# Kernel tuning notes

Measured on AMD Instinct MI355X. Metric: run time of the kernel, lower is better.

The kernel has to match this reference:

```python
import jax, jax.numpy as jnp
import numpy as np

B, S, D = 1, 2048, 1536
H, HD = 24, 64
WINDOW = 512
N_ANCHORS = 4
THETA = 10000.0


def _rope(x):
    # x: [B, H, S, hd] -- matches torch code applied on (B*H, S, hd) with offset=0
    hd = x.shape[-1]
    inv_freq = 1.0 / (THETA ** (jnp.arange(0, hd, 2, dtype=jnp.float32) / hd))
    t = jnp.arange(x.shape[2], dtype=jnp.float32)
    freqs = jnp.outer(t, inv_freq)                      # [S, hd//2]
    emb = jnp.concatenate([freqs, freqs], axis=-1)      # [S, hd]
    cos, sin = jnp.cos(emb), jnp.sin(emb)
    x_rot = jnp.concatenate([-x[..., hd // 2:], x[..., : hd // 2]], axis=-1)
    return x * cos + x_rot * sin


def setup_inputs() -> dict:
    key = jax.random.key(0)
    kx, km, kq, kk, kv = jax.random.split(key, 5)
    std = 0.02
    return {
        "x": jax.random.normal(kx, (B, S, D), jnp.float32),
        "spike_mask": jax.random.bernoulli(km, 0.5, (B, S)),
        "Wq": jax.random.normal(kq, (D, D), jnp.float32) * std,
        "Wk": jax.random.normal(kk, (D, D), jnp.float32) * std,
        "Wv": jax.random.normal(kv, (D, D), jnp.float32) * std,
    }


def reference(x, spike_mask, Wq, Wk, Wv):
    Bq, Sq, Dd = x.shape
    # QKV projections (nn.Linear, bias=False: y = x @ W.T), split heads -> [B, H, S, hd]
    Q = jnp.einsum('bsd,ed->bse', x, Wq).reshape(Bq, Sq, H, HD).transpose(0, 2, 1, 3)
    K = jnp.einsum('bsd,ed->bse', x, Wk).reshape(Bq, Sq, H, HD).transpose(0, 2, 1, 3)
    V = jnp.einsum('bsd,ed->bse', x, Wv).reshape(Bq, Sq, H, HD).transpose(0, 2, 1, 3)
    Q = _rope(Q)
    K = _rope(K)

    # structured mask: causal & (within window | global anchor columns)
    pos = jnp.arange(Sq)
    dist = pos[:, None] - pos[None, :]
    attn_mask = (dist >= 0) & ((dist <= WINDOW) | (pos[None, :] < N_ANCHORS))  # [S, S]

    full_mask = attn_mask[None, None] & spike_mask[:, None, None, :]  # [B,1,S,S]
    query_has_any_key = jnp.any(full_mask, axis=-1, keepdims=True)    # [B,1,S,1]
    safe_mask = full_mask | ~query_has_any_key

    scale = HD ** -0.5
    scores = jnp.einsum('bhqd,bhkd->bhqk', Q, K) * scale
    weights = jax.nn.softmax(jnp.where(safe_mask, scores, -jnp.inf), axis=-1)
    out = jnp.einsum('bhqk,bhkd->bhqd', weights, V)
    out = jnp.where(query_has_any_key, out, 0.0)

    out = out.transpose(0, 2, 1, 3).reshape(Bq, Sq, Dd)
    return out * spike_mask[..., None].astype(out.dtype)
```

## Files before the change

### kernel.cpp

```cpp
#include <hip/hip_runtime.h>
#include <cstdint>
#include <cstddef>

#define S_LEN   2048
#define D_MODEL 1536
#define NH      24
#define HDIM    64
#define WINDOW  512
#define NANCH   4

typedef __attribute__((ext_vector_type(8))) short short8;
typedef __attribute__((ext_vector_type(4))) float floatx4;

#define ASYNC_COPY16(g, l) \
    __builtin_amdgcn_global_load_lds((const __attribute__((address_space(1))) uint32_t*)(g), \
                                     (__attribute__((address_space(3))) uint32_t*)(l), 16, 0, 0)

static __device__ __forceinline__ ushort f32_to_bf16(float f) {
    uint32_t u = __float_as_uint(f);
    uint32_t r = (u + 0x7FFFu + ((u >> 16) & 1u)) >> 16;
    return (ushort)r;
}

__global__ __launch_bounds__(256) void convert_prep_kernel(
    const float* __restrict__ x,
    const float* __restrict__ wq, const float* __restrict__ wk, const float* __restrict__ wv,
    const uint8_t* __restrict__ raw,
    ushort* __restrict__ xb, ushort* __restrict__ wb,
    float* __restrict__ normf, float* __restrict__ cs,
    int xq4, int wq4) {
    const int which = blockIdx.y;
    if (which == 4) {
        if (blockIdx.x < 256) {
            int idx = blockIdx.x * 256 + threadIdx.x;
            int s = idx >> 5, i = idx & 31;
            float inv_freq = expf(-(float)i * 0.2878231366242557f);
            float c, sn;
            sincosf((float)s * inv_freq, &sn, &c);
            cs[s * 64 + i]      = c;
            cs[s * 64 + 32 + i] = sn;
            return;
        }
        if (blockIdx.x != 256) return;
        __shared__ int sh[2];
        if (threadIdx.x == 0) { sh[0] = 0; sh[1] = 0; }
        __syncthreads();
        int f = 0, nz = 0;
        for (int i = threadIdx.x; i < S_LEN; i += 256) {
            uint8_t b = raw[i];
            if ((i & 3) == 3 && b == 0x3f) f++;
            if ((i & 3) != 0 && b != 0)    nz++;
        }
        if (f)  atomicAdd(&sh[0], f);
        if (nz) atomicAdd(&sh[1], nz);
        __syncthreads();
        const int mode = (sh[0] > 0) ? 2 : ((sh[1] > 0) ? 1 : 0);
        for (int i = threadIdx.x; i < S_LEN; i += 256) {
            int v;
            if (mode == 2)      v = (((const float*)raw)[i] != 0.0f) ? 1 : 0;
            else if (mode == 1) v = raw[i] ? 1 : 0;
            else                v = (((const int*)raw)[i] != 0) ? 1 : 0;
            normf[i] = v ? 1.0f : 0.0f;
        }
        return;
    }
    const size_t w_elems = (size_t)D_MODEL * D_MODEL;
    const float* src; ushort* dst; int n4;
    if (which == 0)      { src = x;  dst = xb;               n4 = xq4; }
    else if (which == 1) { src = wq; dst = wb;               n4 = wq4; }
    else if (which == 2) { src = wk; dst = wb + w_elems;     n4 = wq4; }
    else                 { src = wv; dst = wb + 2 * w_elems; n4 = wq4; }
    int i = blockIdx.x * blockDim.x + threadIdx.x;
    if (i >= n4) return;
    float4 v = ((const float4*)src)[i];
    ushort4 o;
    o.x = f32_to_bf16(v.x);
    o.y = f32_to_bf16(v.y);
    o.z = f32_to_bf16(v.z);
    o.w = f32_to_bf16(v.w);
    ((ushort4*)dst)[i] = o;
}

__global__ __launch_bounds__(256) void gemm_qkv_kernel(
    const ushort* __restrict__ xb,
    const ushort* __restrict__ wb,
    const float*  __restrict__ cs,
    ushort* __restrict__ Qf, ushort* __restrict__ Kf, ushort* __restrict__ Vf)
{
    const int lb  = blockIdx.x;
    const int idx = (lb & 7) * 72 + (lb >> 3);
    const int z   = idx / 192;
    const int rem = idx % 192;
    const int n2  = rem >> 4;
    const int tm  = rem & 15;
    const ushort* W = wb + (size_t)z * (D_MODEL * (size_t)D_MODEL);

    __shared__ __align__(16) char smem[32768];

    const int tid  = threadIdx.x;
    const int wave = tid >> 6;
    const int lane = tid & 63;

    const int scol = ((lane & 3) ^ ((lane >> 3) & 3)) * 8;
    const int arow = wave * 32 + (lane >> 2);
    const ushort* gA0 = xb + (size_t)(tm * 128 + arow) * D_MODEL + scol;
    const ushort* gA1 = gA0 + (size_t)16 * D_MODEL;
    const ushort* gB0 = W  + (size_t)(n2 * 128 + arow) * D_MODEL + scol;
    const ushort* gB1 = gB0 + (size_t)16 * D_MODEL;

    const int wm = (wave >> 1) * 64;
    const int wn = (wave & 1) * 64;
    const int lrow  = lane & 15;
    const int quad  = lane >> 4;
    const int xq = (quad ^ ((lrow >> 1) & 3)) * 8;

    floatx4 acc[4][4];
#pragma unroll
    for (int i = 0; i < 4; ++i)
#pragma unroll
        for (int j = 0; j < 4; ++j)
            acc[i][j] = (floatx4){0.f, 0.f, 0.f, 0.f};

    auto STAGE = [&](int b, int kt) {
        ushort* lA = (ushort*)(smem + b * 16384) + wave * 1024;
        ushort* lB = lA + 4096;
        const int ko = kt * 32;
        ASYNC_COPY16(gA0 + ko, lA);
        ASYNC_COPY16(gA1 + ko, lA + 512);
        ASYNC_COPY16(gB0 + ko, lB);
        ASYNC_COPY16(gB1 + ko, lB + 512);
    };

    auto COMPUTE = [&](int b) {
        const ushort* Ah = (const ushort*)(smem + b * 16384);
        const ushort* Bh = Ah + 4096;
        short8 af[4], bf[4];
#pragma unroll
        for (int i = 0; i < 4; ++i) af[i] = *(const short8*)(&Ah[(wm + i * 16 + lrow) * 32 + xq]);
#pragma unroll
        for (int j = 0; j < 4; ++j) bf[j] = *(const short8*)(&Bh[(wn + j * 16 + lrow) * 32 + xq]);
#pragma unroll
        for (int i = 0; i < 4; ++i)
#pragma unroll
            for (int j = 0; j < 4; ++j)
                acc[i][j] = __builtin_amdgcn_mfma_f32_16x16x32_bf16(af[i], bf[j], acc[i][j], 0, 0, 0);
    };

    STAGE(0, 0);
    __syncthreads();

    int cur = 0;
    for (int kt = 0; kt < D_MODEL / 32 - 1; ++kt) {
        STAGE(cur ^ 1, kt + 1);
        COMPUTE(cur);
        __syncthreads();
        cur ^= 1;
    }
    COMPUTE(cur);

    __syncthreads();
    ushort* Lw = (ushort*)(smem + wave * 5120);

    const int r0 = (lane >> 4) * 4;
    const int c0 = lane & 15;
    const int l16  = lane & 15;
    const int h  = n2 * 2 + (wave & 1);
    const int s0 = tm * 128 + wm;

    if (z < 2) {
        const float qscale = (z == 0) ? 0.18033688011112042f : 1.0f;
        ushort* O = (z == 0) ? Qf : Kf;
#pragma unroll
        for (int cc = 0; cc < 2; ++cc) {
#pragma unroll
            for (int i2 = 0; i2 < 2; ++i2) {
                const int i = cc * 2 + i2;
#pragma unroll
                for (int jj = 0; jj < 2; ++jj) {
                    const int cl = jj * 16 + c0;
#pragma unroll
                    for (int r = 0; r < 4; ++r) {
                        const int row = s0 + i * 16 + r0 + r;
                        const float c  = cs[row * 64 + cl];
                        const float sn = cs[row * 64 + 32 + cl];
                        const float x0 = acc[i][jj][r];
                        const float x1 = acc[i][jj + 2][r];
                        const int rl = i2 * 16 + r0 + r;
                        Lw[rl * 72 + cl]      = f32_to_bf16((x0 * c - x1 * sn) * qscale);
                        Lw[rl * 72 + cl + 32] = f32_to_bf16((x1 * c + x0 * sn) * qscale);
                    }
                }
            }
            const int t16base = tm * 8 + (wave >> 1) * 4 + cc * 2;
#pragma unroll
            for (int t = 0; t < 2; ++t) {
#pragma unroll
                for (int p = 0; p < 2; ++p) {
                    uint4 v = *(uint4*)&Lw[(t * 16 + l16) * 72 + p * 32 + quad * 8];
                    *(uint4*)&O[((((size_t)h * 128 + t16base + t) * 2 + p) * 64 + lane) * 8] = v;
                }
            }
            if (cc == 0) __syncthreads();
        }
    } else {
#pragma unroll
        for (int cc = 0; cc < 2; ++cc) {
#pragma unroll
            for (int i2 = 0; i2 < 2; ++i2) {
                const int i = cc * 2 + i2;
#pragma unroll
                for (int j = 0; j < 4; ++j) {
                    const int dl = j * 16 + c0;
                    ushort4 o;
                    o.x = f32_to_bf16(acc[i][j][0]);
                    o.y = f32_to_bf16(acc[i][j][1]);
                    o.z = f32_to_bf16(acc[i][j][2]);
                    o.w = f32_to_bf16(acc[i][j][3]);
                    *(ushort4*)&Lw[dl * 40 + i2 * 16 + r0] = o;
                }
            }
            const int kc = tm * 4 + (wave >> 1) * 2 + cc;
#pragma unroll
            for (int j2 = 0; j2 < 4; ++j2) {
                uint4 v = *(uint4*)&Lw[(j2 * 16 + l16) * 40 + quad * 8];
                *(uint4*)&Vf[((((size_t)h * 64 + kc) * 4 + j2) * 64 + lane) * 8] = v;
            }
            if (cc == 0) __syncthreads();
        }
    }
}

__global__ __launch_bounds__(256) void flash_attn_kernel(
    const ushort* __restrict__ Qf,
    const ushort* __restrict__ Kf,
    const ushort* __restrict__ Vf,
    const float* __restrict__ spikef,
    float* __restrict__ out)
{
    const int lb   = blockIdx.x + (blockIdx.y << 7);
    const int h    = (lb & 7) * 3 + ((lb >> 3) >> 7);
    const int qt16 = (lb >> 3) & 127;
    const int qs   = qt16 * 16;
    const int tid  = threadIdx.x;
    const int wid  = tid >> 6;
    const int lane = tid & 63;
    const int quad = lane >> 4;
    const int l16  = lane & 15;

    __shared__ __align__(16) char smem[4 * 4608];
    char* wreg = smem + wid * 4608;
    ushort* Pst = (ushort*)wreg;

    const ushort* Qp = Qf + (((size_t)h * 128 + qt16) * 2) * 512 + lane * 8;
    const short8 qf0 = *(const short8*)(Qp);
    const short8 qf1 = *(const short8*)(Qp + 512);

    const int q_lane = qs + l16;

    float lsum = 0.f;
    floatx4 Oacc[4];
#pragma unroll
    for (int j2 = 0; j2 < 4; ++j2) Oacc[j2] = (floatx4){0.f, 0.f, 0.f, 0.f};

    const int qtt = (qs + 15) >> 6;
    const int lo = (qs > WINDOW ? qs - WINDOW : 0) >> 6;
    const int has_anchor = (lo > 0) ? 1 : 0;
    const int nt = (qtt - lo + 1) + has_anchor;

    const ushort* Kh = Kf + ((size_t)h * 128) * 1024 + lane * 8;
    const ushort* Vh = Vf + ((size_t)h * 64) * 2048 + lane * 8;

    for (int it = wid; it < nt; it += 4) {
        const int t = has_anchor ? (it == 0 ? 0 : lo + it - 1) : it;
        const int mode = (t == qtt) ? 1 : ((has_anchor && t == 0) ? 3 :
                         ((qs + 15 - t * 64 > WINDOW) ? 2 : 0));

        floatx4 S[4];
        float4 sp[4];
#pragma unroll
        for (int f = 0; f < 4; ++f) {
            const int t16 = t * 4 + f;
            const ushort* Kp = Kh + (size_t)t16 * 1024;
            short8 kf0 = *(const short8*)(Kp);
            short8 kf1 = *(const short8*)(Kp + 512);
            sp[f] = *(const float4*)(spikef + t16 * 16 + quad * 4);
            floatx4 a = (floatx4){0.f, 0.f, 0.f, 0.f};
            a = __builtin_amdgcn_mfma_f32_16x16x32_bf16(kf0, qf0, a, 0, 0, 0);
            a = __builtin_amdgcn_mfma_f32_16x16x32_bf16(kf1, qf1, a, 0, 0, 0);
            S[f] = a;
        }

#pragma unroll
        for (int f = 0; f < 4; ++f) {
            const int kb = t * 64 + f * 16 + quad * 4;
#pragma unroll
            for (int r = 0; r < 4; ++r) {
                const int k = kb + r;
                float v;
                if (mode == 0)      v = 1.f;
                else if (mode == 1) v = (k <= q_lane) ? 1.f : 0.f;
                else if (mode == 2) v = ((k >= q_lane - WINDOW) || (k < NANCH)) ? 1.f : 0.f;
                else                v = (k < NANCH) ? 1.f : 0.f;
                const float sv = (r == 0) ? sp[f].x : (r == 1) ? sp[f].y : (r == 2) ? sp[f].z : sp[f].w;
                const float w = exp2f(S[f][r]) * v * sv;
                S[f][r] = w;
                lsum += w;
            }
        }

#pragma unroll
        for (int f = 0; f < 4; ++f) {
            uint32_t p01 = (__float_as_uint(S[f][0]) >> 16) | (__float_as_uint(S[f][1]) & 0xFFFF0000u);
            uint32_t p23 = (__float_as_uint(S[f][2]) >> 16) | (__float_as_uint(S[f][3]) & 0xFFFF0000u);
            uint2 pk; pk.x = p01; pk.y = p23;
            *(uint2*)(Pst + l16 * 72 + f * 16 + quad * 4) = pk;
        }

#pragma unroll
        for (int c = 0; c < 2; ++c) {
            const short8 pA = *(const short8*)(Pst + l16 * 72 + c * 32 + quad * 8);
            const int kc = t * 2 + c;
#pragma unroll
            for (int j2 = 0; j2 < 4; ++j2) {
                const short8 vf = *(const short8*)(Vh + (size_t)kc * 2048 + j2 * 512);
                Oacc[j2] = __builtin_amdgcn_mfma_f32_16x16x32_bf16(pA, vf, Oacc[j2], 0, 0, 0);
            }
        }
    }

#pragma unroll
    for (int j2 = 0; j2 < 4; ++j2)
        *(floatx4*)(wreg + j2 * 1024 + lane * 16) = Oacc[j2];
    *(float*)(wreg + 4096 + lane * 4) = lsum;
    __syncthreads();

    floatx4 Os = (floatx4){0.f, 0.f, 0.f, 0.f};
    float lt = 0.f;
#pragma unroll
    for (int w = 0; w < 4; ++w) {
        Os += *(const floatx4*)(smem + w * 4608 + wid * 1024 + lane * 16);
        lt += *(const float*)(smem + w * 4608 + 4096 + lane * 4);
    }
    lt += __shfl_xor(lt, 16);
    lt += __shfl_xor(lt, 32);

#pragma unroll
    for (int r = 0; r < 4; ++r) {
        const float lr = __int_as_float(__builtin_amdgcn_ds_bpermute((quad * 4 + r) * 4,
                                                                     __float_as_int(lt)));
        const int qrow = qs + quad * 4 + r;
        const float linv = (lr > 0.f && spikef[qrow] != 0.f) ? (1.0f / lr) : 0.f;
        out[(size_t)qrow * D_MODEL + h * HDIM + wid * 16 + l16] = Os[r] * linv;
    }
}

extern "C" void kernel_launch(void* const* d_in, const int* in_sizes, int n_in,
                              void* d_out, int out_size, void* d_ws, size_t ws_size,
                              hipStream_t stream) {
    const float* x     = (const float*)d_in[0];
    const uint8_t* spike_raw = (const uint8_t*)d_in[1];
    const float* Wq    = (const float*)d_in[2];
    const float* Wk    = (const float*)d_in[3];
    const float* Wv    = (const float*)d_in[4];
    float* out = (float*)d_out;

    const size_t xb_elems = (size_t)S_LEN * D_MODEL;
    const size_t w_elems  = (size_t)D_MODEL * D_MODEL;
    const size_t hs_elems = (size_t)NH * S_LEN * HDIM;

    char* ws = (char*)d_ws;
    size_t off = 0;
    ushort* xb = (ushort*)(ws + off); off += xb_elems * 2;
    ushort* wb = (ushort*)(ws + off); off += 3 * w_elems * 2;
    ushort* Qf = (ushort*)(ws + off); off += hs_elems * 2;
    ushort* Kf = (ushort*)(ws + off); off += hs_elems * 2;
    ushort* Vf = (ushort*)(ws + off); off += hs_elems * 2;
    float*  cst = (float*)(ws + off); off += (size_t)S_LEN * 64 * 4;
    float* spike_f = (float*)(ws + off); off += S_LEN * 4;
    if (ws_size < off) return;

    {
        int xq4 = (int)(xb_elems / 4);
        int wq4 = (int)(w_elems / 4);
        convert_prep_kernel<<<dim3(3072, 5), 256, 0, stream>>>(
            x, Wq, Wk, Wv, spike_raw, xb, wb, spike_f, cst, xq4, wq4);
    }

    gemm_qkv_kernel<<<576, 256, 0, stream>>>(xb, wb, cst, Qf, Kf, Vf);

    flash_attn_kernel<<<dim3(128, 24), 256, 0, stream>>>(Qf, Kf, Vf, spike_f, out);
}
```

Measured before the change: 176.9 us.

## Split QKV GEMM tile across 8 waves instead of 4

The QKV projection GEMM now launches 512 threads per block, with each of 8 waves computing a 32x64 sub-tile instead of 64x64. Each wave issues one async copy each for A and B per k-step, and the epilogue is serialized into two wave groups that share LDS staging with a barrier between them. This halves per-wave accumulator registers and raises the number of waves available to hide latency, but adds block-level synchronization and lowers MFMA work per LDS fragment load.

```diff
diff --git a/kernel.cpp b/kernel.cpp
--- a/kernel.cpp
+++ b/kernel.cpp
@@ -81,7 +81,7 @@
     ((ushort4*)dst)[i] = o;
 }
 
-__global__ __launch_bounds__(256) void gemm_qkv_kernel(
+__global__ __launch_bounds__(512) void gemm_qkv_kernel(
     const ushort* __restrict__ xb,
     const ushort* __restrict__ wb,
     const float*  __restrict__ cs,
@@ -102,45 +102,40 @@
     const int lane = tid & 63;
 
     const int scol = ((lane & 3) ^ ((lane >> 3) & 3)) * 8;
-    const int arow = wave * 32 + (lane >> 2);
-    const ushort* gA0 = xb + (size_t)(tm * 128 + arow) * D_MODEL + scol;
-    const ushort* gA1 = gA0 + (size_t)16 * D_MODEL;
-    const ushort* gB0 = W  + (size_t)(n2 * 128 + arow) * D_MODEL + scol;
-    const ushort* gB1 = gB0 + (size_t)16 * D_MODEL;
-
-    const int wm = (wave >> 1) * 64;
+    const int srow = wave * 16 + (lane >> 2);
+    const ushort* gA = xb + (size_t)(tm * 128 + srow) * D_MODEL + scol;
+    const ushort* gB = W  + (size_t)(n2 * 128 + srow) * D_MODEL + scol;
+
+    const int wm = (wave >> 1) * 32;
     const int wn = (wave & 1) * 64;
     const int lrow  = lane & 15;
     const int quad  = lane >> 4;
     const int xq = (quad ^ ((lrow >> 1) & 3)) * 8;
 
-    floatx4 acc[4][4];
-#pragma unroll
-    for (int i = 0; i < 4; ++i)
+    floatx4 acc[2][4];
+#pragma unroll
+    for (int i = 0; i < 2; ++i)
 #pragma unroll
         for (int j = 0; j < 4; ++j)
             acc[i][j] = (floatx4){0.f, 0.f, 0.f, 0.f};
 
     auto STAGE = [&](int b, int kt) {
-        ushort* lA = (ushort*)(smem + b * 16384) + wave * 1024;
-        ushort* lB = lA + 4096;
+        ushort* l = (ushort*)(smem + b * 16384) + wave * 512;
         const int ko = kt * 32;
-        ASYNC_COPY16(gA0 + ko, lA);
-        ASYNC_COPY16(gA1 + ko, lA + 512);
-        ASYNC_COPY16(gB0 + ko, lB);
-        ASYNC_COPY16(gB1 + ko, lB + 512);
+        ASYNC_COPY16(gA + ko, l);
+        ASYNC_COPY16(gB + ko, l + 4096);
     };
 
     auto COMPUTE = [&](int b) {
         const ushort* Ah = (const ushort*)(smem + b * 16384);
         const ushort* Bh = Ah + 4096;
-        short8 af[4], bf[4];
-#pragma unroll
-        for (int i = 0; i < 4; ++i) af[i] = *(const short8*)(&Ah[(wm + i * 16 + lrow) * 32 + xq]);
+        short8 af[2], bf[4];
+#pragma unroll
+        for (int i = 0; i < 2; ++i) af[i] = *(const short8*)(&Ah[(wm + i * 16 + lrow) * 32 + xq]);
 #pragma unroll
         for (int j = 0; j < 4; ++j) bf[j] = *(const short8*)(&Bh[(wn + j * 16 + lrow) * 32 + xq]);
 #pragma unroll
-        for (int i = 0; i < 4; ++i)
+        for (int i = 0; i < 2; ++i)
 #pragma unroll
             for (int j = 0; j < 4; ++j)
                 acc[i][j] = __builtin_amdgcn_mfma_f32_16x16x32_bf16(af[i], bf[j], acc[i][j], 0, 0, 0);
@@ -159,7 +154,6 @@
     COMPUTE(cur);
 
     __syncthreads();
-    ushort* Lw = (ushort*)(smem + wave * 5120);
 
     const int r0 = (lane >> 4) * 4;
     const int c0 = lane & 15;
@@ -167,66 +161,63 @@
     const int h  = n2 * 2 + (wave & 1);
     const int s0 = tm * 128 + wm;
 
-    if (z < 2) {
-        const float qscale = (z == 0) ? 0.18033688011112042f : 1.0f;
-        ushort* O = (z == 0) ? Qf : Kf;
-#pragma unroll
-        for (int cc = 0; cc < 2; ++cc) {
-#pragma unroll
-            for (int i2 = 0; i2 < 2; ++i2) {
-                const int i = cc * 2 + i2;
-#pragma unroll
-                for (int jj = 0; jj < 2; ++jj) {
-                    const int cl = jj * 16 + c0;
-#pragma unroll
-                    for (int r = 0; r < 4; ++r) {
-                        const int row = s0 + i * 16 + r0 + r;
-                        const float c  = cs[row * 64 + cl];
-                        const float sn = cs[row * 64 + 32 + cl];
-                        const float x0 = acc[i][jj][r];
-                        const float x1 = acc[i][jj + 2][r];
-                        const int rl = i2 * 16 + r0 + r;
-                        Lw[rl * 72 + cl]      = f32_to_bf16((x0 * c - x1 * sn) * qscale);
-                        Lw[rl * 72 + cl + 32] = f32_to_bf16((x1 * c + x0 * sn) * qscale);
+#pragma unroll
+    for (int g = 0; g < 2; ++g) {
+        if ((wave >> 2) == g) {
+            ushort* Lw = (ushort*)(smem + (wave & 3) * 8192);
+            if (z < 2) {
+                const float qscale = (z == 0) ? 0.18033688011112042f : 1.0f;
+                ushort* O = (z == 0) ? Qf : Kf;
+#pragma unroll
+                for (int i = 0; i < 2; ++i) {
+#pragma unroll
+                    for (int jj = 0; jj < 2; ++jj) {
+                        const int cl = jj * 16 + c0;
+#pragma unroll
+                        for (int r = 0; r < 4; ++r) {
+                            const int row = s0 + i * 16 + r0 + r;
+                            const float c  = cs[row * 64 + cl];
+                            const float sn = cs[row * 64 + 32 + cl];
+                            const float x0 = acc[i][jj][r];
+                            const float x1 = acc[i][jj + 2][r];
+                            const int rl = i * 16 + r0 + r;
+                            Lw[rl * 72 + cl]      = f32_to_bf16((x0 * c - x1 * sn) * qscale);
+                            Lw[rl * 72 + cl + 32] = f32_to_bf16((x1 * c + x0 * sn) * qscale);
+                        }
                     }
                 }
-            }
-            const int t16base = tm * 8 + (wave >> 1) * 4 + cc * 2;
-#pragma unroll
-            for (int t = 0; t < 2; ++t) {
-#pragma unroll
-                for (int p = 0; p < 2; ++p) {
-                    uint4 v = *(uint4*)&Lw[(t * 16 + l16) * 72 + p * 32 + quad * 8];
-                    *(uint4*)&O[((((size_t)h * 128 + t16base + t) * 2 + p) * 64 + lane) * 8] = v;
+                const int t16base = tm * 8 + (wave >> 1) * 2;
+#pragma unroll
+                for (int t = 0; t < 2; ++t) {
+#pragma unroll
+                    for (int p = 0; p < 2; ++p) {
+                        uint4 v = *(uint4*)&Lw[(t * 16 + l16) * 72 + p * 32 + quad * 8];
+                        *(uint4*)&O[((((size_t)h * 128 + t16base + t) * 2 + p) * 64 + lane) * 8] = v;
+                    }
+                }
+            } else {
+#pragma unroll
+                for (int i = 0; i < 2; ++i) {
+#pragma unroll
+                    for (int j = 0; j < 4; ++j) {
+                        const int dl = j * 16 + c0;
+                        ushort4 o;
+                        o.x = f32_to_bf16(acc[i][j][0]);
+                        o.y = f32_to_bf16(acc[i][j][1]);
+                        o.z = f32_to_bf16(acc[i][j][2]);
+                        o.w = f32_to_bf16(acc[i][j][3]);
+                        *(ushort4*)&Lw[dl * 40 + i * 16 + r0] = o;
+                    }
+                }
+                const int kc = tm * 4 + (wave >> 1);
+#pragma unroll
+                for (int j2 = 0; j2 < 4; ++j2) {
+                    uint4 v = *(uint4*)&Lw[(j2 * 16 + l16) * 40 + quad * 8];
+                    *(uint4*)&Vf[((((size_t)h * 64 + kc) * 4 + j2) * 64 + lane) * 8] = v;
                 }
             }
-            if (cc == 0) __syncthreads();
-        }
-    } else {
-#pragma unroll
-        for (int cc = 0; cc < 2; ++cc) {
-#pragma unroll
-            for (int i2 = 0; i2 < 2; ++i2) {
-                const int i = cc * 2 + i2;
-#pragma unroll
-                for (int j = 0; j < 4; ++j) {
-                    const int dl = j * 16 + c0;
-                    ushort4 o;
-                    o.x = f32_to_bf16(acc[i][j][0]);
-                    o.y = f32_to_bf16(acc[i][j][1]);
-                    o.z = f32_to_bf16(acc[i][j][2]);
-                    o.w = f32_to_bf16(acc[i][j][3]);
-                    *(ushort4*)&Lw[dl * 40 + i2 * 16 + r0] = o;
-                }
-            }
-            const int kc = tm * 4 + (wave >> 1) * 2 + cc;
-#pragma unroll
-            for (int j2 = 0; j2 < 4; ++j2) {
-                uint4 v = *(uint4*)&Lw[(j2 * 16 + l16) * 40 + quad * 8];
-                *(uint4*)&Vf[((((size_t)h * 64 + kc) * 4 + j2) * 64 + lane) * 8] = v;
-            }
-            if (cc == 0) __syncthreads();
-        }
+        }
+        __syncthreads();
     }
 }
 
@@ -386,7 +377,7 @@
             x, Wq, Wk, Wv, spike_raw, xb, wb, spike_f, cst, xq4, wq4);
     }
 
-    gemm_qkv_kernel<<<576, 256, 0, stream>>>(xb, wb, cst, Qf, Kf, Vf);
+    gemm_qkv_kernel<<<576, 512, 0, stream>>>(xb, wb, cst, Qf, Kf, Vf);
 
     flash_attn_kernel<<<dim3(128, 24), 256, 0, stream>>>(Qf, Kf, Vf, spike_f, out);
 }
```

New measurement: 171.7 us (median of 2 runs). 1.03x faster.
